# Kernel optimization log

Hardware: AMD Instinct MI355X
Metric: run time of the kernel (lower is better)

The kernel has to match this reference:

```python
import jax, jax.numpy as jnp
import numpy as np

B, T, C = 2, 1024, 1024
A, N = 1024, 64
H = A // N
I = 3584
E = 8
HASH_PRIME = 5099  # primes[layer_id=0]
LNX_EPS = 1e-5 * 8 * 8  # eps * head_size_divisor**2


def _layer_norm(x, g, b, eps=1e-5):
    m = jnp.mean(x, -1, keepdims=True)
    v = jnp.mean(jnp.square(x - m), -1, keepdims=True)
    return (x - m) * jax.lax.rsqrt(v + eps) * g + b


def _group_norm(x, g, b, groups, eps):
    M, Cc = x.shape
    xg = x.reshape(M, groups, Cc // groups)
    m = jnp.mean(xg, -1, keepdims=True)
    v = jnp.mean(jnp.square(xg - m), -1, keepdims=True)
    xg = (xg - m) * jax.lax.rsqrt(v + eps)
    return xg.reshape(M, Cc) * g + b


def _time_shift(x):  # nn.ZeroPad2d((0,0,1,-1)): shift tokens right by one, zero-pad first
    return jnp.pad(x, ((0, 0), (1, 0), (0, 0)))[:, :-1]


def _wkv(r, k, v, w_raw, u):
    # r,k,v,w_raw: [B,T,H,N]; u: [H,N]. Mirrors rwkv7_moe_linear_attention_cpu.
    w = jnp.exp(-jnp.exp(w_raw))

    def step(s, inp):
        rt, kt, vt, wt = inp  # each [B,H,N]
        kv = kt[..., :, None] * vt[..., None, :]  # rank-1 outer product [B,H,N,N]
        out = jnp.einsum('bhn,bhnm->bhm', rt, u[None, :, :, None] * kv + s)
        s = jax.lax.stop_gradient(kv + wt[..., :, None] * s)  # torch.no_grad() state update
        return s, out

    s0 = jnp.zeros((r.shape[0], H, N, N), r.dtype)
    xs = tuple(jnp.moveaxis(t, 1, 0) for t in (r, k, v, w))
    _, out = jax.lax.scan(step, s0, xs)
    return jnp.moveaxis(out, 0, 1)  # [B,T,H,N]


def _expert(x, wk, wv):  # value(relu(key(x))^2)
    return jnp.square(jax.nn.relu(x @ wk.T)) @ wv.T


def _forward(input_ids, hidden, pre_ln_g, pre_ln_b, ln1_g, ln1_b, ln2_g, ln2_b,
             att_maa_x, att_maa_w, att_maa_k, att_maa_v, att_maa_r, att_maa_g,
             att_maa_w1, att_maa_w2, att_td, att_td_w1, att_td_w2, att_u,
             att_wr, att_wk, att_wv, att_wg, att_wo, lnx_g, lnx_b,
             ffn_maa_k, ffn_maa_r, ffn_wr, sh_wk, sh_wv, ex_wk, ex_wv):
    x = _layer_norm(hidden, pre_ln_g, pre_ln_b)  # layer_id == 0 pre_ln
    # ---- RWKV7 self-attention ----
    h = _layer_norm(x, ln1_g, ln1_b)
    sh = _time_shift(h)
    xx = sh - h
    xxx = h + xx * att_maa_x
    t5 = jnp.tanh(xxx @ att_maa_w1).reshape(B * T, 5, -1).transpose(1, 0, 2)  # [5,BT,32]
    t5 = jnp.einsum('fbd,fdc->fbc', t5, att_maa_w2).reshape(5, B, T, C)
    mw, mk, mv, mr, mg = t5
    r = (h + xx * (att_maa_r + mr)) @ att_wr.T
    k = (h + xx * (att_maa_k + mk)) @ att_wk.T
    v = (h + xx * (att_maa_v + mv)) @ att_wv.T
    g = jax.nn.silu((h + xx * (att_maa_g + mg)) @ att_wg.T)
    td = jnp.tanh((h + xx * (att_maa_w + mw)) @ att_td_w1) @ att_td_w2 + att_td
    out = _wkv(r.reshape(B, T, H, N), k.reshape(B, T, H, N),
               v.reshape(B, T, H, N), td.reshape(B, T, H, N), att_u)
    out = _group_norm(out.reshape(B * T, A), lnx_g, lnx_b, H, LNX_EPS).reshape(B, T, A)
    x = x + (g * out) @ att_wo.T
    # ---- hash-routed MoE feed-forward ----
    h = _layer_norm(x, ln2_g, ln2_b)
    sh = _time_shift(h)
    d = sh - h
    recept = jax.nn.sigmoid((h + d * ffn_maa_r) @ ffn_wr.T)
    flat = (h + d * ffn_maa_k).reshape(B * T, C)
    val = _expert(flat, sh_wk, sh_wv)  # shared expert
    assign = (input_ids.reshape(-1).astype(jnp.int32) * HASH_PRIME) % E
    for e in range(E):  # fixed small expert loop; mask-combine == gather/index_add
        mask = (assign == e).astype(flat.dtype)[:, None]
        val = val + mask * _expert(flat, ex_wk[e], ex_wv[e])
    x = x + recept * val.reshape(B, T, C)
    return x


def setup_inputs() -> dict:
    key = jax.random.key(0)
    it = iter(jax.random.split(key, 40))
    nrm = lambda shape, s: jax.random.normal(next(it), shape, jnp.float32) * s
    inp = {}
    inp['hidden'] = nrm((B, T, C), 1.0)
    inp['input_ids'] = jax.random.randint(next(it), (B, T), 0, 50257)
    for nm in ['pre_ln', 'ln1', 'ln2']:
        inp[nm + '_g'] = 1.0 + nrm((C,), 0.02)
        inp[nm + '_b'] = nrm((C,), 0.02)
    for nm in ['x', 'w', 'k', 'v', 'r', 'g']:
        inp['att_maa_' + nm] = nrm((C,), 0.1)
    inp['att_maa_w1'] = nrm((C, 5 * 32), 0.02)
    inp['att_maa_w2'] = nrm((5, 32, C), 0.02)
    inp['att_td'] = nrm((A,), 0.1)
    inp['att_td_w1'] = nrm((C, 64), 0.02)
    inp['att_td_w2'] = nrm((64, A), 0.02)
    inp['att_u'] = nrm((H, N), 0.1)
    for nm in ['wr', 'wk', 'wv', 'wg']:
        inp['att_' + nm] = nrm((A, C), 0.02)
    inp['att_wo'] = nrm((C, A), 0.02)
    inp['lnx_g'] = 1.0 + nrm((A,), 0.02)
    inp['lnx_b'] = nrm((A,), 0.02)
    inp['ffn_maa_k'] = nrm((C,), 0.1)
    inp['ffn_maa_r'] = nrm((C,), 0.1)
    inp['ffn_wr'] = nrm((C, C), 0.02)
    inp['sh_wk'] = nrm((I, C), 0.02)
    inp['sh_wv'] = nrm((C, I), 0.02)
    inp['ex_wk'] = nrm((E, I, C), 0.02)
    inp['ex_wv'] = nrm((E, C, I), 0.02)
    return inp


def reference(hidden, input_ids, pre_ln_g, pre_ln_b, ln1_g, ln1_b, ln2_g, ln2_b,
              att_maa_x, att_maa_w, att_maa_k, att_maa_v, att_maa_r, att_maa_g,
              att_maa_w1, att_maa_w2, att_td, att_td_w1, att_td_w2, att_u,
              att_wr, att_wk, att_wv, att_wg, att_wo, lnx_g, lnx_b,
              ffn_maa_k, ffn_maa_r, ffn_wr, sh_wk, sh_wv, ex_wk, ex_wv):
    return _forward(input_ids, hidden, pre_ln_g, pre_ln_b, ln1_g, ln1_b, ln2_g, ln2_b,
                    att_maa_x, att_maa_w, att_maa_k, att_maa_v, att_maa_r, att_maa_g,
                    att_maa_w1, att_maa_w2, att_td, att_td_w1, att_td_w2, att_u,
                    att_wr, att_wk, att_wv, att_wg, att_wo, lnx_g, lnx_b,
                    ffn_maa_k, ffn_maa_r, ffn_wr, sh_wk, sh_wv, ex_wk, ex_wv)
```

## Files before the change

### kernel.cpp

```cpp
#include <hip/hip_runtime.h>
#include <hip/hip_bf16.h>

typedef __hip_bfloat16 bf16;

__device__ __forceinline__ float b2f(bf16 x){ return __bfloat162float(x); }
__device__ __forceinline__ bf16  f2b(float x){ return __float2bfloat16(x); }
__device__ __forceinline__ float ldA(const float* p){ return *p; }
__device__ __forceinline__ float ldA(const bf16* p){ return b2f(*p); }

#define BTOK 2048
#define CC 1024
#define AA 1024
#define IDIM 3584
#define NEXP 8
#define CHUNK 64
#define NCHUNK 16
#define MAXTILE 24

typedef __attribute__((ext_vector_type(8))) short   s8v;
typedef __attribute__((ext_vector_type(8))) __bf16  b8v;
typedef __attribute__((ext_vector_type(4))) float   f4v;

__device__ __forceinline__ unsigned short f2bf_bits(float f){
  unsigned u = __builtin_bit_cast(unsigned, f);
  u += 0x7fffu + ((u >> 16) & 1u);
  return (unsigned short)(u >> 16);
}

#define GLDS16(g, l) __builtin_amdgcn_global_load_lds( \
    (const __attribute__((address_space(1))) void*)(g), \
    (__attribute__((address_space(3)))       void*)(l), 16, 0, 0)

__device__ __forceinline__ float block_sum256(float v, float* red){
  #pragma unroll
  for (int o = 32; o > 0; o >>= 1) v += __shfl_down(v, o, 64);
  int lane = threadIdx.x & 63, wid = threadIdx.x >> 6;
  if (lane == 0) red[wid] = v;
  __syncthreads();
  float s = red[0] + red[1] + red[2] + red[3];
  __syncthreads();
  return s;
}

__global__ __launch_bounds__(256) void k_ln_pre(
    const float* __restrict__ hidden,
    const float* __restrict__ g0, const float* __restrict__ b0,
    const float* __restrict__ g1, const float* __restrict__ b1,
    float* __restrict__ xout, float* __restrict__ hout){
  __shared__ float red[8];
  int t = blockIdx.x, tid = threadIdx.x;
  const float* src = hidden + (size_t)t * CC;
  float v[4];
  #pragma unroll
  for (int i = 0; i < 4; ++i) v[i] = src[tid + 256*i];
  float mean = block_sum256(v[0]+v[1]+v[2]+v[3], red) * (1.f/CC);
  float vs = 0.f;
  #pragma unroll
  for (int i = 0; i < 4; ++i){ float d = v[i]-mean; vs += d*d; }
  float var = block_sum256(vs, red) * (1.f/CC);
  float inv = rsqrtf(var + 1e-5f);
  float xv[4];
  #pragma unroll
  for (int i = 0; i < 4; ++i){
    int c = tid + 256*i;
    xv[i] = (v[i]-mean)*inv*g0[c] + b0[c];
    xout[(size_t)t*CC + c] = xv[i];
  }
  float mean2 = block_sum256(xv[0]+xv[1]+xv[2]+xv[3], red) * (1.f/CC);
  vs = 0.f;
  #pragma unroll
  for (int i = 0; i < 4; ++i){ float d = xv[i]-mean2; vs += d*d; }
  float var2 = block_sum256(vs, red) * (1.f/CC);
  float inv2 = rsqrtf(var2 + 1e-5f);
  #pragma unroll
  for (int i = 0; i < 4; ++i){
    int c = tid + 256*i;
    hout[(size_t)t*CC + c] = (xv[i]-mean2)*inv2*g1[c] + b1[c];
  }
}

__global__ __launch_bounds__(256) void k_mix_att(
    const float* __restrict__ h,
    const float* __restrict__ maa_x, const float* __restrict__ w1, const float* __restrict__ w2,
    const float* __restrict__ maa_w, const float* __restrict__ maa_k, const float* __restrict__ maa_v,
    const float* __restrict__ maa_r, const float* __restrict__ maa_g,
    bf16* __restrict__ zw, bf16* __restrict__ zk, bf16* __restrict__ zv,
    bf16* __restrict__ zr, bf16* __restrict__ zg){
  int t = blockIdx.x, tid = threadIdx.x;
  int tb = t & 1023;
  __shared__ float hs[CC], xxs[CC], xxxs[CC], t160[160];
  #pragma unroll
  for (int i = 0; i < 4; ++i){
    int c = tid + 256*i;
    float hv = h[(size_t)t*CC + c];
    float pv = tb ? h[(size_t)(t-1)*CC + c] : 0.f;
    float xx = pv - hv;
    hs[c] = hv; xxs[c] = xx;
    xxxs[c] = hv + xx * maa_x[c];
  }
  __syncthreads();
  if (tid < 160){
    float acc = 0.f;
    for (int c = 0; c < CC; ++c) acc = fmaf(xxxs[c], w1[c*160 + tid], acc);
    t160[tid] = tanhf(acc);
  }
  __syncthreads();
  const float* maas[5] = {maa_w, maa_k, maa_v, maa_r, maa_g};
  bf16* zs[5] = {zw, zk, zv, zr, zg};
  #pragma unroll
  for (int f = 0; f < 5; ++f){
    #pragma unroll
    for (int i = 0; i < 4; ++i){
      int c = tid + 256*i;
      float acc = 0.f;
      #pragma unroll
      for (int d = 0; d < 32; ++d)
        acc = fmaf(t160[f*32 + d], w2[(size_t)(f*32 + d)*CC + c], acc);
      float z = hs[c] + xxs[c] * (maas[f][c] + acc);
      zs[f][(size_t)t*CC + c] = f2b(z);
    }
  }
}

#define BM 64
#define BN 64
#define BK 16
template <typename TA>
__global__ __launch_bounds__(256) void k_gemm(
    const TA* __restrict__ A, const float* __restrict__ W,
    float* __restrict__ Of32, int M, int N, int K, int epi, int kslices){
  __shared__ float As[BK][BM+1];
  __shared__ float Bs[BK][BN+1];
  int bn = blockIdx.x * BN, bm = blockIdx.y * BM;
  int klen = K / kslices;
  int kbeg = blockIdx.z * klen;
  int tid = threadIdx.x;
  int tx = tid & 15, ty = tid >> 4;
  int lr = tid >> 2;
  int lk = (tid & 3) * 4;
  const TA*    Ap = A + (size_t)(bm + lr)*K + lk;
  const float* Wp = W + (size_t)(bn + lr)*K + lk;
  float acc[4][4] = {};
  for (int k0 = kbeg; k0 < kbeg + klen; k0 += BK){
    #pragma unroll
    for (int j = 0; j < 4; ++j){
      As[lk+j][lr] = ldA(Ap + k0 + j);
      Bs[lk+j][lr] = Wp[k0 + j];
    }
    __syncthreads();
    #pragma unroll
    for (int kk = 0; kk < BK; ++kk){
      float av[4], bv[4];
      #pragma unroll
      for (int i = 0; i < 4; ++i) av[i] = As[kk][ty*4 + i];
      #pragma unroll
      for (int j = 0; j < 4; ++j) bv[j] = Bs[kk][tx*4 + j];
      #pragma unroll
      for (int i = 0; i < 4; ++i)
        #pragma unroll
        for (int j = 0; j < 4; ++j) acc[i][j] = fmaf(av[i], bv[j], acc[i][j]);
    }
    __syncthreads();
  }
  #pragma unroll
  for (int i = 0; i < 4; ++i){
    int row = bm + ty*4 + i;
    #pragma unroll
    for (int j = 0; j < 4; ++j){
      int col = bn + tx*4 + j;
      size_t oi = (size_t)row*N + col;
      if (epi == 0) Of32[oi] = acc[i][j];
      else          atomicAdd(Of32 + oi, acc[i][j]);
    }
  }
}

struct MGB { const void* A[4]; const float* W[4]; void* O[4]; };

template<int AF32, int EPI, int SPLITK, int NB>
__global__ __launch_bounds__(256) void k_mg(MGB args, int N, int K){
  constexpr int ABYTES = AF32 ? 16384 : 8192;
  __shared__ char lds[ABYTES + 16384];
  unsigned short* As  = (unsigned short*)lds;
  float*          AsF = (float*)lds;
  float*          BsF = (float*)(lds + ABYTES);

  const int bz = blockIdx.z;
  const int bi = bz / SPLITK, kh = bz % SPLITK;
  const int Kh = K / SPLITK, kbeg = kh * Kh;
  const unsigned short* Ab = (const unsigned short*)args.A[bi];
  const float*          Af = (const float*)args.A[bi];
  const float*          W  = args.W[bi];
  const int bm = blockIdx.y*128, bn = blockIdx.x*128;
  const int tid = threadIdx.x, l = tid & 63, w = tid >> 6;
  const int mr = (w >> 1)*64, nc = (w & 1)*64;
  const int r4 = tid >> 2, c4 = tid & 3;
  const int r8 = tid >> 3, c8 = tid & 7;

  f4v acc[4][4];
  #pragma unroll
  for (int i = 0; i < 4; ++i)
    #pragma unroll
    for (int j = 0; j < 4; ++j){ f4v z = {0.f,0.f,0.f,0.f}; acc[i][j] = z; }

  const int nk = Kh / 32;
  for (int kt = 0; kt < nk; ++kt){
    const int kk = kbeg + kt*32;
    __syncthreads();
    if (!AF32){
      GLDS16(Ab + (size_t)(bm + r4      )*K + kk + c4*8, (char*)As + tid*16);
      GLDS16(Ab + (size_t)(bm + 64 + r4 )*K + kk + c4*8, (char*)As + 4096 + tid*16);
    } else {
      #pragma unroll
      for (int s = 0; s < 4; ++s){
        int r = s*32 + r8, cs = c8 ^ (r & 7);
        GLDS16(Af + (size_t)(bm + r)*K + kk + cs*4, (char*)AsF + s*4096 + tid*16);
      }
    }
    #pragma unroll
    for (int s = 0; s < 4; ++s){
      int r = s*32 + r8, cs = c8 ^ (r & 7);
      GLDS16(W + (size_t)(bn + r)*K + kk + cs*4, (char*)BsF + s*4096 + tid*16);
    }
    __syncthreads();
    b8v afr[4], bfr[4];
    #pragma unroll
    for (int f = 0; f < 4; ++f){
      if (!AF32){
        afr[f] = *(const b8v*)&As[(mr + f*16 + (l&15))*32 + (l>>4)*8];
      } else {
        int row = mr + f*16 + (l&15), s = row & 7, p = (2*(l>>4)) ^ s;
        f4v q0 = *(const f4v*)&AsF[row*32 + p*4];
        f4v q1 = *(const f4v*)&AsF[row*32 + (p^1)*4];
        s8v t;
        #pragma unroll
        for (int j = 0; j < 4; ++j){ t[j] = (short)f2bf_bits(q0[j]); t[4+j] = (short)f2bf_bits(q1[j]); }
        afr[f] = __builtin_bit_cast(b8v, t);
      }
      {
        int row = nc + f*16 + (l&15), s = row & 7, p = (2*(l>>4)) ^ s;
        f4v q0 = *(const f4v*)&BsF[row*32 + p*4];
        f4v q1 = *(const f4v*)&BsF[row*32 + (p^1)*4];
        s8v t;
        #pragma unroll
        for (int j = 0; j < 4; ++j){ t[j] = (short)f2bf_bits(q0[j]); t[4+j] = (short)f2bf_bits(q1[j]); }
        bfr[f] = __builtin_bit_cast(b8v, t);
      }
    }
    #pragma unroll
    for (int fr = 0; fr < 4; ++fr)
      #pragma unroll
      for (int fc = 0; fc < 4; ++fc)
        acc[fr][fc] = __builtin_amdgcn_mfma_f32_16x16x32_bf16(afr[fr], bfr[fc], acc[fr][fc], 0, 0, 0);
  }
  const int rb = bm + mr + ((l >> 4) << 2);
  const int cb = bn + nc + (l & 15);
  #pragma unroll
  for (int fr = 0; fr < 4; ++fr)
    #pragma unroll
    for (int fc = 0; fc < 4; ++fc)
      #pragma unroll
      for (int j = 0; j < 4; ++j){
        size_t oi = (size_t)(rb + fr*16 + j)*N + (cb + fc*16);
        float v = acc[fr][fc][j];
        if (EPI == 0)      ((float*)args.O[bi])[oi] = v;
        else if (EPI == 1){ v = v > 0.f ? v : 0.f; ((unsigned short*)args.O[bi])[oi] = f2bf_bits(v*v); }
        else               atomicAdd((float*)args.O[bi] + oi, v);
      }
}

template<int MODE>
__global__ __launch_bounds__(256) void k_mg_moe(
    const unsigned short* __restrict__ A, const float* __restrict__ Wbase, size_t wstride,
    float* __restrict__ Of32, unsigned short* __restrict__ Obf, int N, int K, int splitk,
    const int* __restrict__ rowmap, const int* __restrict__ counts,
    const int* __restrict__ offsets, const int* __restrict__ tilemap,
    const int* __restrict__ ntilesp){
  const int ti = blockIdx.x;
  if (ti >= *ntilesp) return;
  const int tmv = tilemap[ti];
  const int e = tmv >> 8;
  const int mbase = (tmv & 255) * 128;
  const int cnt = counts[e];
  const int obase = offsets[e];
  const float* W = Wbase + (size_t)e*wstride;
  const int kh = blockIdx.z;
  const int Kh = K / splitk, kbeg = kh * Kh;
  __shared__ char lds[8192 + 16384];
  unsigned short* As  = (unsigned short*)lds;
  float*          BsF = (float*)(lds + 8192);
  const int tid = threadIdx.x, l = tid & 63, w = tid >> 6;
  const int bn = blockIdx.y*128;
  const int mr = (w >> 1)*64, nc = (w & 1)*64;
  const int r4 = tid >> 2, c4 = tid & 3;
  const int r8 = tid >> 3, c8 = tid & 7;

  int grow[2];
  #pragma unroll
  for (int s = 0; s < 2; ++s){
    int lr = mbase + s*64 + r4;
    lr = lr < cnt ? lr : cnt - 1;
    grow[s] = (MODE == 0) ? rowmap[obase + lr] : (obase + lr);
  }

  f4v acc[4][4];
  #pragma unroll
  for (int i = 0; i < 4; ++i)
    #pragma unroll
    for (int j = 0; j < 4; ++j){ f4v z = {0.f,0.f,0.f,0.f}; acc[i][j] = z; }

  const int nk = Kh / 32;
  for (int kt = 0; kt < nk; ++kt){
    const int kk = kbeg + kt*32;
    __syncthreads();
    GLDS16(A + (size_t)grow[0]*K + kk + c4*8, (char*)As + tid*16);
    GLDS16(A + (size_t)grow[1]*K + kk + c4*8, (char*)As + 4096 + tid*16);
    #pragma unroll
    for (int s = 0; s < 4; ++s){
      int r = s*32 + r8, cs = c8 ^ (r & 7);
      GLDS16(W + (size_t)(bn + r)*K + kk + cs*4, (char*)BsF + s*4096 + tid*16);
    }
    __syncthreads();
    b8v afr[4], bfr[4];
    #pragma unroll
    for (int f = 0; f < 4; ++f){
      afr[f] = *(const b8v*)&As[(mr + f*16 + (l&15))*32 + (l>>4)*8];
      int row = nc + f*16 + (l&15), s = row & 7, p = (2*(l>>4)) ^ s;
      f4v q0 = *(const f4v*)&BsF[row*32 + p*4];
      f4v q1 = *(const f4v*)&BsF[row*32 + (p^1)*4];
      s8v t;
      #pragma unroll
      for (int j = 0; j < 4; ++j){ t[j] = (short)f2bf_bits(q0[j]); t[4+j] = (short)f2bf_bits(q1[j]); }
      bfr[f] = __builtin_bit_cast(b8v, t);
    }
    #pragma unroll
    for (int fr = 0; fr < 4; ++fr)
      #pragma unroll
      for (int fc = 0; fc < 4; ++fc)
        acc[fr][fc] = __builtin_amdgcn_mfma_f32_16x16x32_bf16(afr[fr], bfr[fc], acc[fr][fc], 0, 0, 0);
  }
  const int rb = mbase + mr + ((l >> 4) << 2);
  const int cb = bn + nc + (l & 15);
  #pragma unroll
  for (int fr = 0; fr < 4; ++fr)
    #pragma unroll
    for (int fc = 0; fc < 4; ++fc)
      #pragma unroll
      for (int j = 0; j < 4; ++j){
        int lrow = rb + fr*16 + j;
        if (lrow >= cnt) continue;
        int col = cb + fc*16;
        float v = acc[fr][fc][j];
        if (MODE == 0){
          size_t oi = (size_t)(obase + lrow)*N + col;
          v = v > 0.f ? v : 0.f;
          Obf[oi] = f2bf_bits(v*v);
        } else {
          int orow = rowmap[obase + lrow];
          atomicAdd(Of32 + (size_t)orow*N + col, v);
        }
      }
}

__global__ void k_wprep(const float* __restrict__ td, const float* __restrict__ bias,
                        float* __restrict__ wbuf, int n){
  int i = blockIdx.x*256 + threadIdx.x;
  if (i >= n) return;
  wbuf[i] = expf(-expf(td[i] + bias[i & (AA-1)]));
}

__global__ __launch_bounds__(64) void k_wkv_chunk(
    const float* __restrict__ kb, const float* __restrict__ vb,
    const float* __restrict__ wb, float* __restrict__ Bc, float* __restrict__ Ac){
  int blk = blockIdx.x;
  int stream = blk >> 4, c = blk & (NCHUNK-1);
  int b = stream >> 4, hh = stream & 15;
  int lane = threadIdx.x;
  __shared__ float ks[64], ws[64];
  float s[64];
  #pragma unroll
  for (int n = 0; n < 64; ++n) s[n] = 0.f;
  float prod = 1.f;
  int t0 = c * CHUNK;
  for (int tt = 0; tt < CHUNK; ++tt){
    size_t idx = ((size_t)(b*1024 + t0 + tt))*AA + hh*64 + lane;
    float kt = kb[idx], vt = vb[idx], wt = wb[idx];
    __syncthreads();
    ks[lane] = kt; ws[lane] = wt;
    __syncthreads();
    prod *= wt;
    #pragma unroll
    for (int n = 0; n < 64; ++n)
      s[n] = fmaf(ws[n], s[n], ks[n]*vt);
  }
  float* Bp = Bc + ((size_t)stream*NCHUNK + c)*4096;
  #pragma unroll
  for (int n = 0; n < 64; ++n) Bp[n*64 + lane] = s[n];
  Ac[((size_t)stream*NCHUNK + c)*64 + lane] = prod;
}

__global__ __launch_bounds__(64) void k_wkv_combine(
    float* __restrict__ Bc, const float* __restrict__ Ac){
  int stream = blockIdx.x;
  int lane = threadIdx.x;
  __shared__ float as[64];
  float S[64];
  #pragma unroll
  for (int n = 0; n < 64; ++n) S[n] = 0.f;
  for (int c = 0; c < NCHUNK; ++c){
    __syncthreads();
    as[lane] = Ac[((size_t)stream*NCHUNK + c)*64 + lane];
    __syncthreads();
    float* Bp = Bc + ((size_t)stream*NCHUNK + c)*4096;
    #pragma unroll
    for (int n = 0; n < 64; ++n){
      float bcv = Bp[n*64 + lane];
      Bp[n*64 + lane] = S[n];
      S[n] = fmaf(as[n], S[n], bcv);
    }
  }
}

__global__ __launch_bounds__(64) void k_wkv_out(
    const float* __restrict__ rb, const float* __restrict__ kb,
    const float* __restrict__ vb, const float* __restrict__ wb,
    const float* __restrict__ u, const float* __restrict__ Sc,
    float* __restrict__ ob){
  int blk = blockIdx.x;
  int stream = blk >> 4, c = blk & (NCHUNK-1);
  int b = stream >> 4, hh = stream & 15;
  int lane = threadIdx.x;
  __shared__ float rs[64], ks[64], ws[64], us[64];
  us[lane] = u[hh*64 + lane];
  const float* Sp = Sc + ((size_t)stream*NCHUNK + c)*4096;
  float s[64];
  #pragma unroll
  for (int n = 0; n < 64; ++n) s[n] = Sp[n*64 + lane];
  int t0 = c * CHUNK;
  for (int tt = 0; tt < CHUNK; ++tt){
    size_t idx = ((size_t)(b*1024 + t0 + tt))*AA + hh*64 + lane;
    float rt = rb[idx], kt = kb[idx], vt = vb[idx], wt = wb[idx];
    __syncthreads();
    rs[lane] = rt; ks[lane] = kt; ws[lane] = wt;
    __syncthreads();
    float o0 = 0.f, o1 = 0.f;
    #pragma unroll
    for (int n = 0; n < 64; n += 2){
      float kv0 = ks[n]*vt;
      o0 = fmaf(rs[n], fmaf(us[n], kv0, s[n]), o0);
      s[n] = fmaf(ws[n], s[n], kv0);
      float kv1 = ks[n+1]*vt;
      o1 = fmaf(rs[n+1], fmaf(us[n+1], kv1, s[n+1]), o1);
      s[n+1] = fmaf(ws[n+1], s[n+1], kv1);
    }
    ob[idx] = o0 + o1;
  }
}

__global__ __launch_bounds__(256) void k_gnorm_gate(
    const float* __restrict__ ob, const float* __restrict__ gb,
    const float* __restrict__ lg, const float* __restrict__ lb, float* __restrict__ ao){
  int t = blockIdx.x, tid = threadIdx.x;
  int lane = tid & 63, wid = tid >> 6;
  #pragma unroll
  for (int i = 0; i < 4; ++i){
    int head = wid*4 + i;
    int cidx = head*64 + lane;
    size_t idx = (size_t)t*AA + cidx;
    float v = ob[idx];
    float s1 = v, s2 = v*v;
    #pragma unroll
    for (int o = 32; o > 0; o >>= 1){
      s1 += __shfl_xor(s1, o, 64);
      s2 += __shfl_xor(s2, o, 64);
    }
    float m   = s1 * (1.f/64.f);
    float var = s2 * (1.f/64.f) - m*m;
    float nv  = (v - m) * rsqrtf(var + 6.4e-4f) * lg[cidx] + lb[cidx];
    float gv  = gb[idx];
    float gate = gv / (1.f + expf(-gv));
    ao[idx] = nv * gate;
  }
}

__global__ __launch_bounds__(256) void k_ln2mix(
    const float* __restrict__ xr, const float* __restrict__ at,
    const float* __restrict__ g2, const float* __restrict__ b2v,
    const float* __restrict__ fmaa_r, const float* __restrict__ fmaa_k,
    bf16* __restrict__ zfr, bf16* __restrict__ zfk){
  __shared__ float red[8];
  int t = blockIdx.x, tid = threadIdx.x;
  int tb = t & 1023;
  float cur[4], prv[4];
  #pragma unroll
  for (int i = 0; i < 4; ++i){
    int c = tid + 256*i;
    cur[i] = xr[(size_t)t*CC + c] + at[(size_t)t*CC + c];
    prv[i] = tb ? (xr[(size_t)(t-1)*CC + c] + at[(size_t)(t-1)*CC + c]) : 0.f;
  }
  float m1 = block_sum256(cur[0]+cur[1]+cur[2]+cur[3], red) * (1.f/CC);
  float vs = 0.f;
  #pragma unroll
  for (int i = 0; i < 4; ++i){ float d = cur[i]-m1; vs += d*d; }
  float inv1 = rsqrtf(block_sum256(vs, red)*(1.f/CC) + 1e-5f);
  float m2 = block_sum256(prv[0]+prv[1]+prv[2]+prv[3], red) * (1.f/CC);
  vs = 0.f;
  #pragma unroll
  for (int i = 0; i < 4; ++i){ float d = prv[i]-m2; vs += d*d; }
  float inv2 = rsqrtf(block_sum256(vs, red)*(1.f/CC) + 1e-5f);
  #pragma unroll
  for (int i = 0; i < 4; ++i){
    int c = tid + 256*i;
    float hc = (cur[i]-m1)*inv1*g2[c] + b2v[c];
    float hp = tb ? ((prv[i]-m2)*inv2*g2[c] + b2v[c]) : 0.f;
    float d = hp - hc;
    zfr[(size_t)t*CC + c] = f2b(hc + d * fmaa_r[c]);
    zfk[(size_t)t*CC + c] = f2b(hc + d * fmaa_k[c]);
  }
}

__global__ __launch_bounds__(512) void k_route(
    const int* __restrict__ ids, int* __restrict__ rowmap,
    int* __restrict__ counts, int* __restrict__ offsets,
    int* __restrict__ tilemap, int* __restrict__ ntilesp){
  int wid = threadIdx.x >> 6, lane = threadIdx.x & 63;
  int e = wid;
  __shared__ int cnt_s[8];
  int c = 0;
  for (int t0 = 0; t0 < BTOK; t0 += 64){
    int a = (ids[t0 + lane] * 5099) & 7;
    unsigned long long m = __ballot(a == e);
    c += __popcll(m);
  }
  if (lane == 0) cnt_s[e] = c;
  __syncthreads();
  int off = 0;
  for (int i = 0; i < e; ++i) off += cnt_s[i];
  if (lane == 0){ counts[e] = cnt_s[e]; offsets[e] = off; }
  if (threadIdx.x == 0){
    int nt = 0;
    for (int ee = 0; ee < 8; ++ee){
      int nct = (cnt_s[ee] + 127) >> 7;
      for (int xt = 0; xt < nct; ++xt) tilemap[nt++] = (ee << 8) | xt;
    }
    *ntilesp = nt;
  }
  int pos = off;
  for (int t0 = 0; t0 < BTOK; t0 += 64){
    int t = t0 + lane;
    int a = (ids[t] * 5099) & 7;
    unsigned long long m = __ballot(a == e);
    if (a == e){
      int r = __popcll(m & ((1ull << lane) - 1ull));
      rowmap[pos + r] = t;
    }
    pos += __popcll(m);
  }
}

__global__ void k_tanh_f(const float* __restrict__ in, float* __restrict__ out, int n){
  int i = blockIdx.x*256 + threadIdx.x;
  if (i >= n) return;
  out[i] = tanhf(in[i]);
}
__global__ void k_transpose_f(const float* __restrict__ in, float* __restrict__ out, int R, int Ccol){
  int idx = blockIdx.x*256 + threadIdx.x;
  if (idx >= R*Ccol) return;
  int r = idx / Ccol, c = idx % Ccol;
  out[c*R + r] = in[idx];
}
__global__ void k_zero(float* __restrict__ p, int n4){
  int i = blockIdx.x*256 + threadIdx.x;
  if (i >= n4) return;
  f4v z = {0.f,0.f,0.f,0.f};
  ((f4v*)p)[i] = z;
}
__global__ void k_final(const float* __restrict__ xr, const float* __restrict__ at,
                        const float* __restrict__ rr, const float* __restrict__ val,
                        float* __restrict__ out, int n){
  int i = blockIdx.x*256 + threadIdx.x;
  if (i >= n) return;
  float r = 1.f / (1.f + expf(-rr[i]));
  out[i] = xr[i] + at[i] + r*val[i];
}

extern "C" void kernel_launch(void* const* d_in, const int* in_sizes, int n_in,
                              void* d_out, int out_size, void* d_ws, size_t ws_size,
                              hipStream_t stream) {
  const float* hidden  = (const float*)d_in[0];
  const int*   ids     = (const int*)  d_in[1];
  const float* pre_g   = (const float*)d_in[2];
  const float* pre_b   = (const float*)d_in[3];
  const float* ln1_g   = (const float*)d_in[4];
  const float* ln1_b   = (const float*)d_in[5];
  const float* ln2_g   = (const float*)d_in[6];
  const float* ln2_b   = (const float*)d_in[7];
  const float* maa_x   = (const float*)d_in[8];
  const float* maa_w   = (const float*)d_in[9];
  const float* maa_k   = (const float*)d_in[10];
  const float* maa_v   = (const float*)d_in[11];
  const float* maa_r   = (const float*)d_in[12];
  const float* maa_g   = (const float*)d_in[13];
  const float* maa_w1  = (const float*)d_in[14];
  const float* maa_w2  = (const float*)d_in[15];
  const float* att_td  = (const float*)d_in[16];
  const float* td_w1   = (const float*)d_in[17];
  const float* td_w2   = (const float*)d_in[18];
  const float* att_u   = (const float*)d_in[19];
  const float* att_wr  = (const float*)d_in[20];
  const float* att_wk  = (const float*)d_in[21];
  const float* att_wv  = (const float*)d_in[22];
  const float* att_wg  = (const float*)d_in[23];
  const float* att_wo  = (const float*)d_in[24];
  const float* lnx_g   = (const float*)d_in[25];
  const float* lnx_b   = (const float*)d_in[26];
  const float* fmaa_k  = (const float*)d_in[27];
  const float* fmaa_r  = (const float*)d_in[28];
  const float* ffn_wr  = (const float*)d_in[29];
  const float* sh_wk   = (const float*)d_in[30];
  const float* sh_wv   = (const float*)d_in[31];
  const float* ex_wk   = (const float*)d_in[32];
  const float* ex_wv   = (const float*)d_in[33];
  (void)ws_size; (void)n_in; (void)in_sizes; (void)out_size;

  char* base = (char*)d_ws;
  const size_t MiB = 1024ull*1024ull;
  float* x      = (float*)(base + 0*MiB);
  float* h      = (float*)(base + 8*MiB);
  float* rbuf   = h;
  float* kbuf   = (float*)(base + 16*MiB);
  float* vbuf   = (float*)(base + 24*MiB);
  unsigned short* hk2 = (unsigned short*)(base + 16*MiB);
  int*   rowmap = (int*)(base + 31*MiB);
  int*   counts = rowmap + BTOK;
  int*   offsets= counts + 64;
  int*   tilemap= offsets + 64;
  int*   ntilesp= tilemap + 64;
  float* gbuf   = (float*)(base + 32*MiB);
  float* val    = gbuf;
  bf16*  zw     = (bf16*)(base + 40*MiB);
  bf16*  zk     = (bf16*)(base + 44*MiB);
  float* tdbuf  = (float*)(base + 40*MiB);
  float* Ac     = (float*)(base + 40*MiB);
  float* wkvout = (float*)(base + 40*MiB);
  float* attout = (float*)(base + 40*MiB);
  bf16*  zr     = (bf16*)(base + 48*MiB);
  bf16*  zg     = (bf16*)(base + 52*MiB);
  float* wbuf   = (float*)(base + 48*MiB);
  float* ao     = (float*)(base + 48*MiB);
  float* recraw = (float*)(base + 48*MiB);
  bf16*  zv     = (bf16*)(base + 56*MiB);
  float* tdw1T  = (float*)(base + 60*MiB);
  float* tdw2T  = (float*)(base + 60*MiB + 256*1024);
  float* tmp64  = (float*)(base + 60*MiB + 512*1024);
  float* tanh64 = (float*)(base + 61*MiB);
  float* chunkS = (float*)(base + 56*MiB);
  bf16*  zfr    = (bf16*)(base + 56*MiB);
  bf16*  zfk    = (bf16*)(base + 60*MiB);

  k_ln_pre<<<BTOK, 256, 0, stream>>>(hidden, pre_g, pre_b, ln1_g, ln1_b, x, h);
  k_mix_att<<<BTOK, 256, 0, stream>>>(h, maa_x, maa_w1, maa_w2,
                                      maa_w, maa_k, maa_v, maa_r, maa_g,
                                      zw, zk, zv, zr, zg);
  {
    MGB a{};
    a.A[0]=zr; a.A[1]=zk; a.A[2]=zv; a.A[3]=zg;
    a.W[0]=att_wr; a.W[1]=att_wk; a.W[2]=att_wv; a.W[3]=att_wg;
    a.O[0]=rbuf; a.O[1]=kbuf; a.O[2]=vbuf; a.O[3]=gbuf;
    k_mg<0,0,1,4><<<dim3(CC/128, BTOK/128, 4), 256, 0, stream>>>(a, AA, CC);
  }
  k_transpose_f<<<(CC*64 + 255)/256, 256, 0, stream>>>(td_w1, tdw1T, CC, 64);
  k_transpose_f<<<(64*AA + 255)/256, 256, 0, stream>>>(td_w2, tdw2T, 64, AA);
  k_zero<<<(BTOK*64/4 + 255)/256, 256, 0, stream>>>(tmp64, BTOK*64/4);
  k_gemm<bf16><<<dim3(1, BTOK/BM, 8), 256, 0, stream>>>(zw, tdw1T, tmp64, BTOK, 64, CC, 2, 8);
  k_tanh_f<<<(BTOK*64 + 255)/256, 256, 0, stream>>>(tmp64, tanh64, BTOK*64);
  k_gemm<float><<<dim3(AA/BN, BTOK/BM, 1), 256, 0, stream>>>(tanh64, tdw2T, tdbuf, BTOK, AA, 64, 0, 1);
  k_wprep<<<(BTOK*AA + 255)/256, 256, 0, stream>>>(tdbuf, att_td, wbuf, BTOK*AA);
  k_wkv_chunk<<<32*NCHUNK, 64, 0, stream>>>(kbuf, vbuf, wbuf, chunkS, Ac);
  k_wkv_combine<<<32, 64, 0, stream>>>(chunkS, Ac);
  k_wkv_out<<<32*NCHUNK, 64, 0, stream>>>(rbuf, kbuf, vbuf, wbuf, att_u, chunkS, wkvout);
  k_gnorm_gate<<<BTOK, 256, 0, stream>>>(wkvout, gbuf, lnx_g, lnx_b, ao);
  k_zero<<<(BTOK*CC/4 + 255)/256, 256, 0, stream>>>(attout, BTOK*CC/4);
  {
    MGB a{}; a.A[0]=ao; a.W[0]=att_wo; a.O[0]=attout;
    k_mg<1,2,2,1><<<dim3(CC/128, BTOK/128, 2), 256, 0, stream>>>(a, CC, AA);
  }
  k_zero<<<(BTOK*CC/4 + 255)/256, 256, 0, stream>>>(recraw, BTOK*CC/4);
  k_ln2mix<<<BTOK, 256, 0, stream>>>(x, attout, ln2_g, ln2_b, fmaa_r, fmaa_k, zfr, zfk);
  {
    MGB a{}; a.A[0]=zfr; a.W[0]=ffn_wr; a.O[0]=recraw;
    k_mg<0,2,2,1><<<dim3(CC/128, BTOK/128, 2), 256, 0, stream>>>(a, CC, CC);
  }
  {
    MGB a{}; a.A[0]=zfk; a.W[0]=sh_wk; a.O[0]=hk2;
    k_mg<0,1,1,1><<<dim3(IDIM/128, BTOK/128, 1), 256, 0, stream>>>(a, IDIM, CC);
  }
  k_zero<<<(BTOK*CC/4 + 255)/256, 256, 0, stream>>>(val, BTOK*CC/4);
  {
    MGB a{}; a.A[0]=hk2; a.W[0]=sh_wv; a.O[0]=val;
    k_mg<0,2,2,1><<<dim3(CC/128, BTOK/128, 2), 256, 0, stream>>>(a, CC, IDIM);
  }
  k_route<<<1, 512, 0, stream>>>(ids, rowmap, counts, offsets, tilemap, ntilesp);
  k_mg_moe<0><<<dim3(MAXTILE, IDIM/128, 1), 256, 0, stream>>>(
      (const unsigned short*)zfk, ex_wk, (size_t)IDIM*CC, nullptr, hk2, IDIM, CC, 1,
      rowmap, counts, offsets, tilemap, ntilesp);
  k_mg_moe<1><<<dim3(MAXTILE, CC/128, 2), 256, 0, stream>>>(
      hk2, ex_wv, (size_t)CC*IDIM, val, nullptr, CC, IDIM, 2,
      rowmap, counts, offsets, tilemap, ntilesp);
  k_final<<<(BTOK*CC + 255)/256, 256, 0, stream>>>(x, attout, recraw, val, (float*)d_out, BTOK*CC);
}
```

Baseline: 1.119 ms.

## Split token-mix kernel into bf16 MFMA GEMM plus batched w2 mixing

```diff
diff --git a/kernel.cpp b/kernel.cpp
--- a/kernel.cpp
+++ b/kernel.cpp
@@ -79,45 +79,66 @@
   }
 }
 
-__global__ __launch_bounds__(256) void k_mix_att(
-    const float* __restrict__ h,
-    const float* __restrict__ maa_x, const float* __restrict__ w1, const float* __restrict__ w2,
+__global__ __launch_bounds__(256) void k_mix_xxx(
+    const float* __restrict__ h, const float* __restrict__ maa_x,
+    bf16* __restrict__ zxx){
+  int t = blockIdx.x, tid = threadIdx.x;
+  int tb = t & 1023;
+  #pragma unroll
+  for (int i = 0; i < 4; ++i){
+    int c = tid + 256*i;
+    float hv = h[(size_t)t*CC + c];
+    float pv = tb ? h[(size_t)(t-1)*CC + c] : 0.f;
+    zxx[(size_t)t*CC + c] = f2b(hv + (pv - hv) * maa_x[c]);
+  }
+}
+
+__global__ __launch_bounds__(256) void k_tanh160(
+    const float* __restrict__ in, float* __restrict__ out){
+  int t = blockIdx.x, j = threadIdx.x;
+  if (j < 160) out[(size_t)t*160 + j] = tanhf(in[(size_t)t*256 + j]);
+}
+
+__global__ __launch_bounds__(256) void k_mix_out(
+    const float* __restrict__ h, const float* __restrict__ t160g,
+    const float* __restrict__ w2,
     const float* __restrict__ maa_w, const float* __restrict__ maa_k, const float* __restrict__ maa_v,
     const float* __restrict__ maa_r, const float* __restrict__ maa_g,
     bf16* __restrict__ zw, bf16* __restrict__ zk, bf16* __restrict__ zv,
     bf16* __restrict__ zr, bf16* __restrict__ zg){
-  int t = blockIdx.x, tid = threadIdx.x;
-  int tb = t & 1023;
-  __shared__ float hs[CC], xxs[CC], xxxs[CC], t160[160];
-  #pragma unroll
-  for (int i = 0; i < 4; ++i){
-    int c = tid + 256*i;
-    float hv = h[(size_t)t*CC + c];
-    float pv = tb ? h[(size_t)(t-1)*CC + c] : 0.f;
-    float xx = pv - hv;
-    hs[c] = hv; xxs[c] = xx;
-    xxxs[c] = hv + xx * maa_x[c];
-  }
-  __syncthreads();
-  if (tid < 160){
-    float acc = 0.f;
-    for (int c = 0; c < CC; ++c) acc = fmaf(xxxs[c], w1[c*160 + tid], acc);
-    t160[tid] = tanhf(acc);
-  }
+  int t0 = blockIdx.x * 4, tid = threadIdx.x;
+  __shared__ float ts[640];
+  for (int j = tid; j < 640; j += 256) ts[j] = t160g[(size_t)t0*160 + j];
   __syncthreads();
   const float* maas[5] = {maa_w, maa_k, maa_v, maa_r, maa_g};
   bf16* zs[5] = {zw, zk, zv, zr, zg};
   #pragma unroll
-  for (int f = 0; f < 5; ++f){
-    #pragma unroll
-    for (int i = 0; i < 4; ++i){
-      int c = tid + 256*i;
-      float acc = 0.f;
-      #pragma unroll
-      for (int d = 0; d < 32; ++d)
-        acc = fmaf(t160[f*32 + d], w2[(size_t)(f*32 + d)*CC + c], acc);
-      float z = hs[c] + xxs[c] * (maas[f][c] + acc);
-      zs[f][(size_t)t*CC + c] = f2b(z);
+  for (int i = 0; i < 4; ++i){
+    int c = tid + 256*i;
+    float hv[4], xx[4];
+    #pragma unroll
+    for (int tk = 0; tk < 4; ++tk){
+      int t = t0 + tk, tb = t & 1023;
+      float hvv = h[(size_t)t*CC + c];
+      float pv = tb ? h[(size_t)(t-1)*CC + c] : 0.f;
+      hv[tk] = hvv; xx[tk] = pv - hvv;
+    }
+    #pragma unroll
+    for (int f = 0; f < 5; ++f){
+      float mf = maas[f][c];
+      float a0 = 0.f, a1 = 0.f, a2 = 0.f, a3 = 0.f;
+      #pragma unroll
+      for (int d = 0; d < 32; ++d){
+        float w2v = w2[(size_t)(f*32 + d)*CC + c];
+        a0 = fmaf(ts[  0 + f*32 + d], w2v, a0);
+        a1 = fmaf(ts[160 + f*32 + d], w2v, a1);
+        a2 = fmaf(ts[320 + f*32 + d], w2v, a2);
+        a3 = fmaf(ts[480 + f*32 + d], w2v, a3);
+      }
+      zs[f][(size_t)(t0+0)*CC + c] = f2b(hv[0] + xx[0]*(mf + a0));
+      zs[f][(size_t)(t0+1)*CC + c] = f2b(hv[1] + xx[1]*(mf + a1));
+      zs[f][(size_t)(t0+2)*CC + c] = f2b(hv[2] + xx[2]*(mf + a2));
+      zs[f][(size_t)(t0+3)*CC + c] = f2b(hv[3] + xx[3]*(mf + a3));
     }
   }
 }
@@ -631,6 +652,10 @@
   float* kbuf   = (float*)(base + 16*MiB);
   float* vbuf   = (float*)(base + 24*MiB);
   unsigned short* hk2 = (unsigned short*)(base + 16*MiB);
+  float* w1Tp   = (float*)(base + 16*MiB);
+  float* tmp256 = (float*)(base + 17*MiB);
+  float* t160g  = (float*)(base + 19*MiB);
+  bf16*  zxx    = (bf16*) (base + 20*MiB + 512*1024);
   int*   rowmap = (int*)(base + 31*MiB);
   int*   counts = rowmap + BTOK;
   int*   offsets= counts + 64;
@@ -659,9 +684,18 @@
   bf16*  zfk    = (bf16*)(base + 60*MiB);
 
   k_ln_pre<<<BTOK, 256, 0, stream>>>(hidden, pre_g, pre_b, ln1_g, ln1_b, x, h);
-  k_mix_att<<<BTOK, 256, 0, stream>>>(h, maa_x, maa_w1, maa_w2,
-                                      maa_w, maa_k, maa_v, maa_r, maa_g,
-                                      zw, zk, zv, zr, zg);
+  k_zero<<<(256*CC/4 + 255)/256, 256, 0, stream>>>(w1Tp, 256*CC/4);
+  k_transpose_f<<<(CC*160 + 255)/256, 256, 0, stream>>>(maa_w1, w1Tp, CC, 160);
+  k_zero<<<(BTOK*256/4 + 255)/256, 256, 0, stream>>>(tmp256, BTOK*256/4);
+  k_mix_xxx<<<BTOK, 256, 0, stream>>>(h, maa_x, zxx);
+  {
+    MGB a{}; a.A[0]=zxx; a.W[0]=w1Tp; a.O[0]=tmp256;
+    k_mg<0,2,8,1><<<dim3(256/128, BTOK/128, 8), 256, 0, stream>>>(a, 256, CC);
+  }
+  k_tanh160<<<BTOK, 256, 0, stream>>>(tmp256, t160g);
+  k_mix_out<<<BTOK/4, 256, 0, stream>>>(h, t160g, maa_w2,
+                                        maa_w, maa_k, maa_v, maa_r, maa_g,
+                                        zw, zk, zv, zr, zg);
   {
     MGB a{};
     a.A[0]=zr; a.A[1]=zk; a.A[2]=zv; a.A[3]=zg;
```

Measured after the change: 1.122 ms. Within noise of the previous version (+0.2%).
